# Performance work log

Hardware: AMD Instinct MI355X
Metric: run time of the kernel (lower is better)

Reference implementation:

```python
import jax, jax.numpy as jnp
import numpy as np


def _conv(x, w, pad):
    return jax.lax.conv_general_dilated(
        x, w, (1, 1), [(pad, pad), (pad, pad)],
        dimension_numbers=('NCHW', 'OIHW', 'NCHW'))


def _avgpool2(x):
    B, C, H, W = x.shape
    return x.reshape(B, C, H // 2, 2, W // 2, 2).mean(axis=(3, 5))


def setup_inputs() -> dict:
    key = jax.random.key(0)
    ks = jax.random.split(key, 10)
    B = 1024
    x = jax.random.uniform(ks[0], (B, 1, 28, 28), jnp.float32)
    # depthwise-separable conv params (in=1 -> depthwise is a plain 3x3 conv)
    dw_w = jax.random.normal(ks[1], (1, 1, 3, 3), jnp.float32) * 0.3
    pw_w = jax.random.normal(ks[2], (32, 1, 1, 1), jnp.float32) * 0.3
    pw_b = jax.random.normal(ks[3], (32,), jnp.float32) * 0.05
    # fixed 4-qubit entangling unitary (real orthogonal 16x16), stand-in for tq.RandomLayer(n_ops=8)
    U = jnp.asarray(np.linalg.qr(np.random.default_rng(0).standard_normal((16, 16)))[0],
                    jnp.float32)
    fus_w = jax.random.normal(ks[4], (128, 36, 3, 3), jnp.float32) * (1.0 / np.sqrt(36 * 9))
    fus_b = jax.random.normal(ks[5], (128,), jnp.float32) * 0.05
    F = 128 * 7 * 7
    cls_w = jax.random.normal(ks[6], (10, F), jnp.float32) * (1.0 / np.sqrt(F))
    cls_b = jax.random.normal(ks[7], (10,), jnp.float32) * 0.05
    reg_w = jax.random.normal(ks[8], (1, F), jnp.float32) * (1.0 / np.sqrt(F))
    reg_b = jax.random.normal(ks[9], (1,), jnp.float32) * 0.05
    return {'x': x, 'dw_w': dw_w, 'pw_w': pw_w, 'pw_b': pw_b, 'U': U,
            'fus_w': fus_w, 'fus_b': fus_b, 'cls_w': cls_w, 'cls_b': cls_b,
            'reg_w': reg_w, 'reg_b': reg_b}


def _quantum_patches(x, U):
    # x: (B,1,28,28) -> 14x14 grid of 2x2 patches, 4 RY angles per patch
    B = x.shape[0]
    p = x.reshape(B, 14, 2, 14, 2).transpose(0, 1, 3, 2, 4).reshape(B, 14, 14, 4)
    h = 0.5 * p
    a = jnp.stack([jnp.cos(h), jnp.sin(h)], axis=-1)       # (B,14,14,4,2)
    # RY-encoded product state |psi> = kron over 4 wires -> 16 real amplitudes
    amp = jnp.einsum('...i,...j,...k,...l->...ijkl',
                     a[..., 0, :], a[..., 1, :], a[..., 2, :], a[..., 3, :]
                     ).reshape(B, 14, 14, 16)
    state = amp @ U.T                                       # entangling layer
    probs = state * state
    idx = jnp.arange(16)
    # PauliZ expectation per wire; wire 0 is the most significant bit
    signs = 1.0 - 2.0 * (((idx[None, :] >> (3 - jnp.arange(4)[:, None])) & 1)
                         .astype(jnp.float32))              # (4,16)
    meas = probs @ signs.T                                  # (B,14,14,4)
    # replicate torch.cat(patches,dim=1).view(B,4,14,14): flat row-major then reshape
    return meas.reshape(B, 14 * 14 * 4).reshape(B, 4, 14, 14)


def reference(x, dw_w, pw_w, pw_b, U, fus_w, fus_b, cls_w, cls_b, reg_w, reg_b):
    B = x.shape[0]
    out_ds = _conv(_conv(x, dw_w, 1), pw_w, 0) + pw_b[None, :, None, None]  # (B,32,28,28)
    out_q = _quantum_patches(x, U)                                          # (B,4,14,14)
    out = jnp.concatenate([_avgpool2(out_ds), out_q], axis=1)               # (B,36,14,14)
    out = jax.nn.relu(_conv(out, fus_w, 1) + fus_b[None, :, None, None])    # (B,128,14,14)
    out = _avgpool2(out)                                                    # (B,128,7,7)
    flat = out.reshape(B, -1)
    logits = flat @ cls_w.T + cls_b
    aux = flat @ reg_w.T + reg_b
    return (logits, aux)
```

## Files before the change

### kernel.cpp

```cpp
#include <hip/hip_runtime.h>
#include <math.h>


typedef __bf16 bf16x8 __attribute__((ext_vector_type(8)));
typedef __bf16 bf16x4 __attribute__((ext_vector_type(4)));
typedef float  f32x16 __attribute__((ext_vector_type(16)));

union Pack8 { __bf16 h[8]; uint4 v; };
union QPair { struct { bf16x4 lo, hi; } p; bf16x8 v; };

__global__ __launch_bounds__(256) void prep(
    const float* __restrict__ fus_w,
    const float* __restrict__ cls_w,
    const float* __restrict__ reg_w,
    __bf16* __restrict__ bfrag,
    float* __restrict__ clsTT)
{
    const int gid = blockIdx.x * 256 + threadIdx.x;
    if (gid < 43008) {
        const int j    = gid & 7;
        const int frag = gid >> 3;
        const int lane = frag & 63;
        const int rest = frag >> 6;
        const int m  = rest % 21;
        const int nt = rest / 21;
        const int n  = nt * 32 + (lane & 31);
        const int hk = lane >> 5;
        float v;
        if (m < 18) {
            const int t = m >> 1, ks = m & 1;
            const int ic = ks * 16 + hk * 8 + j;
            v = fus_w[n * 324 + ic * 9 + t];
        } else {
            const int ps = m - 18;
            const int k  = hk * 8 + j;
            const int tap = ps * 4 + (k >> 2);
            const int ch  = k & 3;
            v = (tap < 9) ? fus_w[n * 324 + (32 + ch) * 9 + tap] : 0.f;
        }
        bfrag[gid] = (__bf16)v;
    } else if (gid < 43008 + 86016) {
        const int e   = gid - 43008;
        const int kk  = e % 12;
        const int r0  = e / 12;
        const int l31 = r0 & 31;
        const int r1  = r0 >> 5;
        const int hk  = r1 & 1;
        const int r2  = r1 >> 1;
        const int q   = r2 & 3;
        const int r3  = r2 >> 2;
        const int mt  = r3 % 7;
        const int nt  = r3 / 7;
        const int oc   = nt * 32 + l31;
        const int cell = mt * 8 + q * 2 + hk;
        float v = 0.f;
        if (cell < 49 && kk < 11) {
            const int f = oc * 49 + cell;
            v = (kk < 10) ? cls_w[kk * 6272 + f] : reg_w[f];
        }
        clsTT[e] = v;
    }
}

__device__ __forceinline__ void patch_work(
    const int p, const float* __restrict__ xs, __bf16* __restrict__ actT,
    __bf16* __restrict__ Qt,
    const float* __restrict__ dw_w, const float* __restrict__ pw_w,
    const float* __restrict__ pw_b, const float* __restrict__ U)
{
    if (p >= 196) return;
    const int i = p / 14, j = p % 14;
    const int Y = 2 * i, X = 2 * j;

    float w9[9];
    #pragma unroll
    for (int t = 0; t < 9; ++t) w9[t] = dw_w[t];
    float dsum = 0.f;
    #pragma unroll
    for (int dy = 0; dy < 2; ++dy) {
        #pragma unroll
        for (int dx = 0; dx < 2; ++dx) {
            const int cy = Y + dy, cx = X + dx;
            #pragma unroll
            for (int ky = 0; ky < 3; ++ky) {
                const int yy = cy + ky - 1;
                if (yy < 0 || yy > 27) continue;
                #pragma unroll
                for (int kx = 0; kx < 3; ++kx) {
                    const int xx = cx + kx - 1;
                    if (xx < 0 || xx > 27) continue;
                    dsum += xs[yy * 29 + xx] * w9[ky * 3 + kx];
                }
            }
        }
    }
    const float dpool = 0.25f * dsum;

    const int sp_o = (i + 1) * 16 + (j + 1);
    #pragma unroll
    for (int c8 = 0; c8 < 4; ++c8) {
        Pack8 pk;
        #pragma unroll
        for (int e = 0; e < 8; ++e)
            pk.h[e] = (__bf16)(pw_w[c8 * 8 + e] * dpool + pw_b[c8 * 8 + e]);
        ((uint4*)actT)[sp_o * 5 + c8] = pk.v;
    }

    const float p0 = xs[Y * 29 + X],       p1 = xs[Y * 29 + X + 1];
    const float p2 = xs[(Y + 1) * 29 + X], p3 = xs[(Y + 1) * 29 + X + 1];
    const float s0 = __sinf(0.5f * p0), c0 = __cosf(0.5f * p0);
    const float s1 = __sinf(0.5f * p1), c1 = __cosf(0.5f * p1);
    const float s2 = __sinf(0.5f * p2), c2 = __cosf(0.5f * p2);
    const float s3 = __sinf(0.5f * p3), c3 = __cosf(0.5f * p3);
    float a01[4] = {c0 * c1, c0 * s1, s0 * c1, s0 * s1};
    float a23[4] = {c2 * c3, c2 * s3, s2 * c3, s2 * s3};
    float amp[16];
    #pragma unroll
    for (int hi = 0; hi < 4; ++hi)
        #pragma unroll
        for (int lo = 0; lo < 4; ++lo)
            amp[hi * 4 + lo] = a01[hi] * a23[lo];

    float meas[4] = {0.f, 0.f, 0.f, 0.f};
    #pragma unroll
    for (int m = 0; m < 16; ++m) {
        float st = 0.f;
        #pragma unroll
        for (int n = 0; n < 16; ++n) st = fmaf(U[m * 16 + n], amp[n], st);
        const float pm = st * st;
        meas[0] += ((m >> 3) & 1) ? -pm : pm;
        meas[1] += ((m >> 2) & 1) ? -pm : pm;
        meas[2] += ((m >> 1) & 1) ? -pm : pm;
        meas[3] += (m & 1) ? -pm : pm;
    }
    const int fbase = i * 56 + j * 4;
    #pragma unroll
    for (int w = 0; w < 4; ++w) {
        const int f  = fbase + w;
        const int ch = f / 196;
        const int sp = f - ch * 196;
        const int r2 = sp / 14 + 1, c2i = sp % 14 + 1;
        const int sp2 = r2 * 16 + c2i;
        Qt[sp2 * 4 + ch] = (__bf16)meas[w];
    }
}

__device__ __forceinline__ void conv_fold(
    const __bf16* __restrict__ actT, const __bf16* __restrict__ Qt,
    const bf16x8* __restrict__ bfr, const float4* __restrict__ cls4,
    const float fb_l, const int l31, const int hk,
    const int* __restrict__ offL, const int* __restrict__ offH,
    float* __restrict__ a11)
{
    for (int mt = 0; mt < 7; ++mt) {
        const int mp   = mt * 32 + l31;
        const int cell = mp >> 2;
        const int cc = (cell < 49) ? cell : 48;
        const int py = (cc * 9363) >> 16;
        const int px = cc - py * 7;
        const int yy = 2 * py + ((mp >> 1) & 1);
        const int xx = 2 * px + (mp & 1);
        const int rowbase = yy * 16 + xx;

        f32x16 acc = {0.f,0.f,0.f,0.f,0.f,0.f,0.f,0.f,
                      0.f,0.f,0.f,0.f,0.f,0.f,0.f,0.f};

        #pragma unroll
        for (int t = 0; t < 9; ++t) {
            const int ky = t / 3, kx = t - ky * 3;
            const int row = rowbase + ky * 16 + kx;
            const __bf16* rp = actT + row * 40 + hk * 8;
            #pragma unroll
            for (int ks = 0; ks < 2; ++ks) {
                const bf16x8 af = *(const bf16x8*)(rp + ks * 16);
                acc = __builtin_amdgcn_mfma_f32_32x32x16_bf16(af, bfr[t * 2 + ks],
                                                              acc, 0, 0, 0);
            }
        }
        #pragma unroll
        for (int ps = 0; ps < 3; ++ps) {
            QPair u;
            u.p.lo = *(const bf16x4*)(Qt + (rowbase + offL[ps]) * 4);
            u.p.hi = *(const bf16x4*)(Qt + (rowbase + offH[ps]) * 4);
            acc = __builtin_amdgcn_mfma_f32_32x32x16_bf16(u.v, bfr[18 + ps],
                                                          acc, 0, 0, 0);
        }

        const float4* cwm = cls4 + mt * 768;
        #pragma unroll
        for (int q = 0; q < 4; ++q) {
            float pv = 0.f;
            #pragma unroll
            for (int s = 0; s < 4; ++s) {
                const float v = acc[q * 4 + s] + fb_l;
                pv += (v > 0.f ? v : 0.f);
            }
            pv *= 0.25f;
            const float4 w0 = cwm[q * 192 + 0];
            const float4 w1 = cwm[q * 192 + 1];
            const float4 w2 = cwm[q * 192 + 2];
            a11[0]  = fmaf(pv, w0.x, a11[0]);
            a11[1]  = fmaf(pv, w0.y, a11[1]);
            a11[2]  = fmaf(pv, w0.z, a11[2]);
            a11[3]  = fmaf(pv, w0.w, a11[3]);
            a11[4]  = fmaf(pv, w1.x, a11[4]);
            a11[5]  = fmaf(pv, w1.y, a11[5]);
            a11[6]  = fmaf(pv, w1.z, a11[6]);
            a11[7]  = fmaf(pv, w1.w, a11[7]);
            a11[8]  = fmaf(pv, w2.x, a11[8]);
            a11[9]  = fmaf(pv, w2.y, a11[9]);
            a11[10] = fmaf(pv, w2.z, a11[10]);
        }
    }
}

__global__ __launch_bounds__(256, 2) void quanv_fused(
    const float* __restrict__ x,
    const float* __restrict__ dw_w,
    const float* __restrict__ pw_w,
    const float* __restrict__ pw_b,
    const float* __restrict__ U,
    const __bf16* __restrict__ bfrag,
    const float* __restrict__ fus_b,
    const float* __restrict__ clsTT,
    const float* __restrict__ cls_b,
    const float* __restrict__ reg_b,
    float* __restrict__ out,
    int B)
{
    __shared__ __align__(16) __bf16 actT[2][256 * 40];
    __shared__ __align__(16) __bf16 Qt[2][256 * 4];
    __shared__ float xs[2][812];
    __shared__ float red[2][48];

    const int b0  = blockIdx.x * 2;
    const int b1  = b0 + 1;
    const bool two = (b1 < B);
    const int tid = threadIdx.x;

    {
        uint4 z; z.x = 0; z.y = 0; z.z = 0; z.w = 0;
        uint4* a4 = (uint4*)&actT[0][0];
        for (int i = tid; i < 2560; i += 256) a4[i] = z;
        uint4* q4 = (uint4*)&Qt[0][0];
        if (tid < 256) q4[tid] = z;
        const float* xb = x + (size_t)b0 * 784;
        const int tot = two ? 1568 : 784;
        for (int i = tid; i < tot; i += 256) {
            const int img = i / 784, r = i - img * 784;
            xs[img][r + r / 28] = xb[i];
        }
    }

    const int lane = tid & 63, nt = tid >> 6;
    const int l31  = lane & 31, hk = lane >> 5;
    const float fb_l = fus_b[nt * 32 + l31];
    const int pidx = (lane < 49) ? nt * 49 + lane : 999;

    bf16x8 bfr[21];
    {
        const bf16x8* __restrict__ bp = ((const bf16x8*)bfrag) + (nt * 21 * 64 + lane);
        #pragma unroll
        for (int m = 0; m < 21; ++m) bfr[m] = bp[m * 64];
    }

    int offL[3], offH[3];
    #pragma unroll
    for (int ps = 0; ps < 3; ++ps) {
        int tL = ps * 4 + hk * 2;
        int tH = tL + 1;
        if (tL > 8) tL = 0;
        if (tH > 8) tH = 0;
        offL[ps] = (tL / 3) * 16 + (tL % 3);
        offH[ps] = (tH / 3) * 16 + (tH % 3);
    }

    const float4* __restrict__ cls4 =
        ((const float4*)clsTT) + ((((nt * 7) * 4) * 2 + hk) * 32 + l31) * 3;

    __syncthreads();

    patch_work(pidx, &xs[0][0], &actT[0][0], &Qt[0][0], dw_w, pw_w, pw_b, U);
    __syncthreads();

    float a11_0[11];
    #pragma unroll
    for (int k = 0; k < 11; ++k) a11_0[k] = 0.f;
    if (two) patch_work(pidx, &xs[1][0], &actT[1][0], &Qt[1][0], dw_w, pw_w, pw_b, U);
    conv_fold(&actT[0][0], &Qt[0][0], bfr, cls4, fb_l, l31, hk, offL, offH, a11_0);
    __syncthreads();

    float a11_1[11];
    #pragma unroll
    for (int k = 0; k < 11; ++k) a11_1[k] = 0.f;
    if (two) conv_fold(&actT[1][0], &Qt[1][0], bfr, cls4, fb_l, l31, hk, offL, offH, a11_1);

    #pragma unroll
    for (int k = 0; k < 11; ++k) {
        float a = a11_0[k];
        float c = a11_1[k];
        #pragma unroll
        for (int off = 32; off > 0; off >>= 1) {
            a += __shfl_down(a, off, 64);
            c += __shfl_down(c, off, 64);
        }
        if (lane == 0) { red[0][k * 4 + nt] = a; red[1][k * 4 + nt] = c; }
    }
    __syncthreads();
    if (tid < 11) {
        const float v = red[0][tid * 4] + red[0][tid * 4 + 1]
                      + red[0][tid * 4 + 2] + red[0][tid * 4 + 3];
        if (tid < 10) out[b0 * 10 + tid] = v + cls_b[tid];
        else          out[B * 10 + b0]   = v + reg_b[0];
    } else if (two && tid >= 64 && tid < 75) {
        const int k = tid - 64;
        const float v = red[1][k * 4] + red[1][k * 4 + 1]
                      + red[1][k * 4 + 2] + red[1][k * 4 + 3];
        if (k < 10) out[b1 * 10 + k] = v + cls_b[k];
        else        out[B * 10 + b1] = v + reg_b[0];
    }
}

extern "C" void kernel_launch(void* const* d_in, const int* in_sizes, int n_in,
                              void* d_out, int out_size, void* d_ws, size_t ws_size,
                              hipStream_t stream) {
    const float* x    = (const float*)d_in[0];
    const float* dw_w = (const float*)d_in[1];
    const float* pw_w = (const float*)d_in[2];
    const float* pw_b = (const float*)d_in[3];
    const float* U    = (const float*)d_in[4];
    const float* fw   = (const float*)d_in[5];
    const float* fb   = (const float*)d_in[6];
    const float* cw   = (const float*)d_in[7];
    const float* cb   = (const float*)d_in[8];
    const float* rw   = (const float*)d_in[9];
    const float* rb   = (const float*)d_in[10];
    const int B = in_sizes[0] / 784;

    __bf16* bfrag = (__bf16*)d_ws;
    float*  clsTT = (float*)((char*)d_ws + 86016);

    prep<<<(43008 + 86016 + 255) / 256, 256, 0, stream>>>(fw, cw, rw, bfrag, clsTT);
    const int nblk = (B + 1) / 2;
    quanv_fused<<<nblk, 256, 0, stream>>>(x, dw_w, pw_w, pw_b, U, bfrag, fb,
                                          clsTT, cb, rb, (float*)d_out, B);
}
```

Before: 108.3 us.

## Process one image per block and raise occupancy target to four blocks

The fused kernel now handles a single image per block instead of two. Each block therefore needs half the shared memory, and the launch bound asks for four blocks per CU instead of two. The software overlap between one image's patch work and the other image's conv fold is gone, as is the reuse of the per-block weight-fragment register load across two images. In exchange, more independent blocks can be resident, so the hardware hides latency instead of the manual interleave. The tighter register budget under launch_bounds(256,4) may cause spills of the 21 bf16x8 fragments held in registers.

```diff
diff --git a/kernel.cpp b/kernel.cpp
--- a/kernel.cpp
+++ b/kernel.cpp
@@ -214,7 +214,7 @@
     }
 }
 
-__global__ __launch_bounds__(256, 2) void quanv_fused(
+__global__ __launch_bounds__(256, 4) void quanv_fused(
     const float* __restrict__ x,
     const float* __restrict__ dw_w,
     const float* __restrict__ pw_w,
@@ -228,28 +228,23 @@
     float* __restrict__ out,
     int B)
 {
-    __shared__ __align__(16) __bf16 actT[2][256 * 40];
-    __shared__ __align__(16) __bf16 Qt[2][256 * 4];
-    __shared__ float xs[2][812];
-    __shared__ float red[2][48];
-
-    const int b0  = blockIdx.x * 2;
-    const int b1  = b0 + 1;
-    const bool two = (b1 < B);
+    __shared__ __align__(16) __bf16 actT[256 * 40];
+    __shared__ __align__(16) __bf16 Qt[256 * 4];
+    __shared__ float xs[812];
+    __shared__ float red[48];
+
+    const int b   = blockIdx.x;
     const int tid = threadIdx.x;
 
     {
         uint4 z; z.x = 0; z.y = 0; z.z = 0; z.w = 0;
-        uint4* a4 = (uint4*)&actT[0][0];
-        for (int i = tid; i < 2560; i += 256) a4[i] = z;
-        uint4* q4 = (uint4*)&Qt[0][0];
-        if (tid < 256) q4[tid] = z;
-        const float* xb = x + (size_t)b0 * 784;
-        const int tot = two ? 1568 : 784;
-        for (int i = tid; i < tot; i += 256) {
-            const int img = i / 784, r = i - img * 784;
-            xs[img][r + r / 28] = xb[i];
-        }
+        uint4* a4 = (uint4*)&actT[0];
+        for (int i = tid; i < 1280; i += 256) a4[i] = z;
+        uint4* q4 = (uint4*)&Qt[0];
+        if (tid < 128) q4[tid] = z;
+        const float* xb = x + (size_t)b * 784;
+        for (int i = tid; i < 784; i += 256)
+            xs[i + i / 28] = xb[i];
     }
 
     const int lane = tid & 63, nt = tid >> 6;
@@ -280,44 +275,27 @@
 
     __syncthreads();
 
-    patch_work(pidx, &xs[0][0], &actT[0][0], &Qt[0][0], dw_w, pw_w, pw_b, U);
+    patch_work(pidx, &xs[0], &actT[0], &Qt[0], dw_w, pw_w, pw_b, U);
     __syncthreads();
 
-    float a11_0[11];
-    #pragma unroll
-    for (int k = 0; k < 11; ++k) a11_0[k] = 0.f;
-    if (two) patch_work(pidx, &xs[1][0], &actT[1][0], &Qt[1][0], dw_w, pw_w, pw_b, U);
-    conv_fold(&actT[0][0], &Qt[0][0], bfr, cls4, fb_l, l31, hk, offL, offH, a11_0);
-    __syncthreads();
-
-    float a11_1[11];
-    #pragma unroll
-    for (int k = 0; k < 11; ++k) a11_1[k] = 0.f;
-    if (two) conv_fold(&actT[1][0], &Qt[1][0], bfr, cls4, fb_l, l31, hk, offL, offH, a11_1);
+    float a11[11];
+    #pragma unroll
+    for (int k = 0; k < 11; ++k) a11[k] = 0.f;
+    conv_fold(&actT[0], &Qt[0], bfr, cls4, fb_l, l31, hk, offL, offH, a11);
 
     #pragma unroll
     for (int k = 0; k < 11; ++k) {
-        float a = a11_0[k];
-        float c = a11_1[k];
-        #pragma unroll
-        for (int off = 32; off > 0; off >>= 1) {
-            a += __shfl_down(a, off, 64);
-            c += __shfl_down(c, off, 64);
-        }
-        if (lane == 0) { red[0][k * 4 + nt] = a; red[1][k * 4 + nt] = c; }
+        float a = a11[k];
+        #pragma unroll
+        for (int off = 32; off > 0; off >>= 1) a += __shfl_down(a, off, 64);
+        if (lane == 0) red[k * 4 + nt] = a;
     }
     __syncthreads();
     if (tid < 11) {
-        const float v = red[0][tid * 4] + red[0][tid * 4 + 1]
-                      + red[0][tid * 4 + 2] + red[0][tid * 4 + 3];
-        if (tid < 10) out[b0 * 10 + tid] = v + cls_b[tid];
-        else          out[B * 10 + b0]   = v + reg_b[0];
-    } else if (two && tid >= 64 && tid < 75) {
-        const int k = tid - 64;
-        const float v = red[1][k * 4] + red[1][k * 4 + 1]
-                      + red[1][k * 4 + 2] + red[1][k * 4 + 3];
-        if (k < 10) out[b1 * 10 + k] = v + cls_b[k];
-        else        out[B * 10 + b1] = v + reg_b[0];
+        const float v = red[tid * 4] + red[tid * 4 + 1]
+                      + red[tid * 4 + 2] + red[tid * 4 + 3];
+        if (tid < 10) out[b * 10 + tid] = v + cls_b[tid];
+        else          out[B * 10 + b]   = v + reg_b[0];
     }
 }
 
@@ -341,7 +319,6 @@
     float*  clsTT = (float*)((char*)d_ws + 86016);
 
     prep<<<(43008 + 86016 + 255) / 256, 256, 0, stream>>>(fw, cw, rw, bfrag, clsTT);
-    const int nblk = (B + 1) / 2;
-    quanv_fused<<<nblk, 256, 0, stream>>>(x, dw_w, pw_w, pw_b, U, bfrag, fb,
-                                          clsTT, cb, rb, (float*)d_out, B);
-}
+    quanv_fused<<<B, 256, 0, stream>>>(x, dw_w, pw_w, pw_b, U, bfrag, fb,
+                                       clsTT, cb, rb, (float*)d_out, B);
+}
```

Result: slower. 114.9 us (+6.1%).
